# Performance work log

Hardware: AMD Instinct MI355X
Metric: run time of the kernel (lower is better)

## Reference

```python
import jax, jax.numpy as jnp
import numpy as np

N, E, CS, HE, H = 10000, 160000, 128, 32, 4
S0, V1 = 16, 8          # feat_irreps = 16x0e + 8x1o
QK0, QK1 = 4, 2         # qk_irreps per head = 4x0e + 2x1o
VO0, VO1 = 4, 4         # v_irreps  per head = 4x0e + 4x1o
OK0, OK1 = QK0 * H, QK1 * H     # 16, 8
OV0, OV1 = VO0 * H, VO1 * H     # 16, 16
K_NUMEL = S0*OK0 + V1*OK0 + S0*OK1 + V1*OK1 + V1*OK1   # 640
V_NUMEL = S0*OV0 + V1*OV0 + S0*OV1 + V1*OV1 + V1*OV1   # 896
EPS = 1e-5


def _tp(fs, fv, sh_s, sh_v, w, o0, o1):
    """CG tensor product of (s0 scalars + v1 vectors) with sh=(1x0e+1x1o),
    per-edge weights w (shared_weights=False); outputs o0 scalars + o1 vectors.
    Paths: 0e*0e->0e, 1o.1o->0e (dot), 0e*1o->1o, 1o*0e->1o, 1o x 1o->1o (cross)."""
    s0, v1 = fs.shape[-1], fv.shape[-2]
    i = 0
    ws = []
    for (a, b) in ((s0, o0), (v1, o0), (s0, o1), (v1, o1), (v1, o1)):
        ws.append(w[:, i:i + a * b].reshape(-1, a, b)); i += a * b
    wA, wB, wC, wD, wE = ws
    c0a = jnp.einsum('eu,euw->ew', fs * sh_s[:, None], wA) / np.sqrt(s0)
    dv = jnp.einsum('eui,ei->eu', fv, sh_v)
    c0b = jnp.einsum('eu,euw->ew', dv, wB) / np.sqrt(v1)
    out0 = (c0a + c0b) / np.sqrt(2.0)
    c1c = jnp.einsum('eu,euw->ew', fs, wC)[:, :, None] * sh_v[:, None, :] / np.sqrt(s0)
    c1d = jnp.einsum('eui,euw->ewi', fv, wD) * sh_s[:, None, None] / np.sqrt(v1)
    crs = jnp.cross(fv, sh_v[:, None, :])
    c1e = jnp.einsum('eui,euw->ewi', crs, wE) / np.sqrt(v1)
    out1 = (c1c + c1d + c1e) / np.sqrt(3.0)
    return out0, out1


def _forward(frame_features, rigid_rot, rigid_trans, tfn_features, edge_features, edge_sh,
             W_f0, b_f0, W_f1, b_f1, Wg_s, Wg_v, Wq_s, Wq_v,
             Wk1, bk1, Wk2, bk2, Wv1, bv1, Wv2, bv2,
             Wo_s, Wo_v, Ws_s, Ws_v, bn_ws, bn_bs, bn_wv, edge_index):
    dst, src = edge_index[0], edge_index[1]
    n = tfn_features.shape[0]
    tfn_s = tfn_features[:, :S0]
    tfn_v = tfn_features[:, S0:].reshape(n, V1, 3)
    sh_s, sh_v = edge_sh[:, 0], edge_sh[:, 1:4]

    # frame -> irrep features: 0e via Linear, 1o via Linear + rigid apply
    f0 = frame_features @ W_f0 + b_f0                                   # [N, S0*H]
    f1 = (frame_features @ W_f1 + b_f1).reshape(n, V1 * H, 3)
    f1 = jnp.einsum('nij,nuj->nui', rigid_rot, f1) + rigid_trans[:, None, :]
    gs = f0 @ Wg_s / np.sqrt(f0.shape[-1])                              # o3.Linear 0e -> [N, S0]
    gv = jnp.einsum('nui,uw->nwi', f1, Wg_v) / np.sqrt(f1.shape[1])     # o3.Linear 1o -> [N, V1, 3]

    # queries per node, per head
    q_s = (tfn_s @ Wq_s / np.sqrt(S0)).reshape(n, H, QK0)
    q_v = (jnp.einsum('nui,uw->nwi', tfn_v, Wq_v) / np.sqrt(V1)).reshape(n, H, QK1, 3)

    # per-edge dynamic TP weights from edge features (the big memory term)
    kw = jax.nn.relu(edge_features @ Wk1 + bk1) @ Wk2 + bk2             # [E, 640]
    vw = jax.nn.relu(edge_features @ Wv1 + bv1) @ Wv2 + bv2             # [E, 896]

    fs, fv = gs[dst], gv[dst]                                           # gather at edge_dst
    k_s, k_v = _tp(fs, fv, sh_s, sh_v, kw, OK0, OK1)
    v_s, v_v = _tp(fs, fv, sh_s, sh_v, vw, OV0, OV1)
    k_s = k_s.reshape(-1, H, QK0); k_v = k_v.reshape(-1, H, QK1, 3)
    v_s = v_s.reshape(-1, H, VO0); v_v = v_v.reshape(-1, H, VO1, 3)

    # attention scores + segment softmax over edge_src groups
    attn = jnp.einsum('ehj,ehj->eh', q_s[src], k_s) + jnp.einsum('ehji,ehji->eh', q_v[src], k_v)
    m = jax.ops.segment_max(attn, src, num_segments=n)
    ex = jnp.exp(attn - m[src])
    den = jax.ops.segment_sum(ex, src, num_segments=n)
    alpha = ex / (den[src] + 1e-9)

    upd_s = jax.ops.segment_sum(v_s * alpha[..., None], src, num_segments=n).reshape(n, OV0)
    upd_v = jax.ops.segment_sum(v_v * alpha[..., None, None], src, num_segments=n).reshape(n, OV1, 3)

    out_s = upd_s @ Wo_s / np.sqrt(OV0) + tfn_s @ Ws_s / np.sqrt(S0)
    out_v = jnp.einsum('nui,uw->nwi', upd_v, Wo_v) / np.sqrt(OV1) \
          + jnp.einsum('nui,uw->nwi', tfn_v, Ws_v) / np.sqrt(V1)

    # e3nn-style BatchNorm: scalars mean/var normalized, vectors norm normalized
    mu = out_s.mean(0); xc = out_s - mu
    out_s = xc / jnp.sqrt((xc * xc).mean(0) + EPS) * bn_ws + bn_bs
    n2 = (out_v * out_v).sum(-1).mean(0)
    out_v = out_v / jnp.sqrt(n2 + EPS)[None, :, None] * bn_wv[None, :, None]

    return jnp.concatenate([out_s, out_v.reshape(n, V1 * 3)], axis=-1)   # [N, 40]


def setup_inputs():
    key = jax.random.key(0)
    ks = iter(jax.random.split(key, 40))
    rn = lambda *s: jax.random.normal(next(ks), s, dtype=jnp.float32)
    return dict(
        frame_features=rn(N, CS),
        rigid_rot=rn(N, 3, 3),
        rigid_trans=rn(N, 3),
        tfn_features=rn(N, S0 + 3 * V1),
        edge_features=rn(E, HE),
        edge_sh=rn(E, 4),
        edge_index=jax.random.randint(next(ks), (2, E), 0, N, dtype=jnp.int32),
        W_f0=rn(CS, S0 * H) / np.sqrt(CS), b_f0=jnp.zeros((S0 * H,), jnp.float32),
        W_f1=rn(CS, V1 * H * 3) / np.sqrt(CS), b_f1=jnp.zeros((V1 * H * 3,), jnp.float32),
        Wg_s=rn(S0 * H, S0), Wg_v=rn(V1 * H, V1),
        Wq_s=rn(S0, QK0 * H), Wq_v=rn(V1, QK1 * H),
        Wk1=rn(HE, HE) / np.sqrt(HE), bk1=jnp.zeros((HE,), jnp.float32),
        Wk2=rn(HE, K_NUMEL) / np.sqrt(HE), bk2=jnp.zeros((K_NUMEL,), jnp.float32),
        Wv1=rn(HE, HE) / np.sqrt(HE), bv1=jnp.zeros((HE,), jnp.float32),
        Wv2=rn(HE, V_NUMEL) / np.sqrt(HE), bv2=jnp.zeros((V_NUMEL,), jnp.float32),
        Wo_s=rn(VO0 * H, S0), Wo_v=rn(VO1 * H, V1),
        Ws_s=rn(S0, S0), Ws_v=rn(V1, V1),
        bn_ws=jnp.ones((S0,), jnp.float32), bn_bs=jnp.zeros((S0,), jnp.float32),
        bn_wv=jnp.ones((V1,), jnp.float32),
    )


def reference(frame_features, rigid_rot, rigid_trans, tfn_features, edge_features, edge_sh, edge_index,
              W_f0, b_f0, W_f1, b_f1, Wg_s, Wg_v, Wq_s, Wq_v,
              Wk1, bk1, Wk2, bk2, Wv1, bv1, Wv2, bv2,
              Wo_s, Wo_v, Ws_s, Ws_v, bn_ws, bn_bs, bn_wv):
    return _forward(frame_features, rigid_rot, rigid_trans, tfn_features, edge_features, edge_sh,
                    W_f0, b_f0, W_f1, b_f1, Wg_s, Wg_v, Wq_s, Wq_v,
                    Wk1, bk1, Wk2, bk2, Wv1, bv1, Wv2, bv2,
                    Wo_s, Wo_v, Ws_s, Ws_v, bn_ws, bn_bs, bn_wv, edge_index)
```

## Files before the change

### kernel.cpp

```cpp
#include <hip/hip_runtime.h>
#include <hip/hip_bf16.h>
#include <math.h>

#define NN 10000
#define EE 160000
#define CSZ 128
#define NVB (EE/128)

#define INV_S8  0.35355339059327373f
#define INV_S32 0.17677669529663687f
#define INV_S2  0.7071067811865476f
#define INV_S3  0.5773502691896258f

typedef short s16x8 __attribute__((ext_vector_type(8)));
typedef float f32x4 __attribute__((ext_vector_type(4)));

__device__ __forceinline__ unsigned short f2bf(float f){
  __hip_bfloat16 h = __float2bfloat16(f);
  return *reinterpret_cast<unsigned short*>(&h);
}

__global__ __launch_bounds__(192) void k_node(
    const float* __restrict__ frame,
    const float* __restrict__ Wf0, const float* __restrict__ bf0,
    const float* __restrict__ Wf1, const float* __restrict__ bf1,
    const float* __restrict__ rot, const float* __restrict__ trans,
    const float* __restrict__ tfn,
    const float* __restrict__ Wgs, const float* __restrict__ Wgv,
    const float* __restrict__ Wqs, const float* __restrict__ Wqv,
    float* __restrict__ Gs, float* __restrict__ Gv,
    float* __restrict__ Qs, float* __restrict__ Qv){
  __shared__ float ff[160];
  __shared__ float f1r[32][3];
  int n = blockIdx.x;
  int t = threadIdx.x;
  if(t < 160){
    bool is0 = t < 64;
    int cc = is0 ? t : (t-64);
    const float* W = is0 ? Wf0 : Wf1;
    int ldw = is0 ? 64 : 96;
    float acc = is0 ? bf0[cc] : bf1[cc];
    const float* fp = frame + (size_t)n*CSZ;
    #pragma unroll 8
    for(int k=0;k<CSZ;k++)
      acc = fmaf(fp[k], W[k*ldw + cc], acc);
    ff[t] = acc;
  }
  __syncthreads();
  if(t < 32){
    float v0 = ff[64+t*3+0], v1 = ff[64+t*3+1], v2 = ff[64+t*3+2];
    const float* R = rot + (size_t)n*9;
    const float* tr = trans + (size_t)n*3;
    f1r[t][0] = R[0]*v0 + R[1]*v1 + R[2]*v2 + tr[0];
    f1r[t][1] = R[3]*v0 + R[4]*v1 + R[5]*v2 + tr[1];
    f1r[t][2] = R[6]*v0 + R[7]*v1 + R[8]*v2 + tr[2];
  }
  __syncthreads();
  if(t < 16){
    float a = 0.f;
    #pragma unroll
    for(int u=0;u<64;u++) a = fmaf(ff[u], Wgs[u*16+t], a);
    Gs[(size_t)n*16+t] = a * 0.125f;
  } else if(t < 40){
    int idx = t-16, w = idx/3, i = idx%3; float a = 0.f;
    #pragma unroll
    for(int u=0;u<32;u++) a = fmaf(f1r[u][i], Wgv[u*8+w], a);
    Gv[(size_t)n*24+idx] = a * INV_S32;
  } else if(t < 56){
    int w = t-40; float a = 0.f;
    #pragma unroll
    for(int u=0;u<16;u++) a = fmaf(tfn[(size_t)n*40+u], Wqs[u*16+w], a);
    Qs[(size_t)n*16+w] = a * 0.25f;
  } else if(t < 80){
    int idx = t-56, w = idx/3, i = idx%3; float a = 0.f;
    #pragma unroll
    for(int u=0;u<8;u++) a = fmaf(tfn[(size_t)n*40+16+u*3+i], Wqv[u*8+w], a);
    Qv[(size_t)n*24+idx] = a * INV_S8;
  }
}

__global__ __launch_bounds__(256) void k_hist(const int* __restrict__ ei, int* __restrict__ cnt){
  int e = blockIdx.x*256 + threadIdx.x;
  if(e < EE) atomicAdd(&cnt[ei[EE + e]], 1);
}

__global__ __launch_bounds__(256) void k_scan(const int* __restrict__ cnt,
                                              int* __restrict__ ofs, int* __restrict__ fill){
  __shared__ int tsum[256];
  int t = threadIdx.x;
  const int CH = (NN + 255)/256;
  int base = t*CH;
  int s = 0;
  for(int i=0;i<CH;i++){ int idx=base+i; if(idx<NN) s += cnt[idx]; }
  tsum[t] = s;
  __syncthreads();
  for(int off=1; off<256; off<<=1){
    int v = (t>=off)? tsum[t-off] : 0;
    __syncthreads();
    tsum[t] += v;
    __syncthreads();
  }
  int run = (t==0)? 0 : tsum[t-1];
  for(int i=0;i<CH;i++){
    int idx = base+i;
    if(idx < NN){ ofs[idx] = run; fill[idx] = run; run += cnt[idx]; }
  }
  if(t==255) ofs[NN] = tsum[255];
}

__global__ __launch_bounds__(256) void k_scatter(const int* __restrict__ ei,
                                                 int* __restrict__ fill, int* __restrict__ elist){
  int e = blockIdx.x*256 + threadIdx.x;
  if(e >= EE) return;
  int src = ei[EE + e];
  int pos = atomicAdd(&fill[src], 1);
  elist[pos] = e;
}

__global__ __launch_bounds__(256) void k_prepw(
    const float* __restrict__ Wk2, const float* __restrict__ bk2,
    const float* __restrict__ Wv2, const float* __restrict__ bv2,
    unsigned short* __restrict__ A2rK, unsigned short* __restrict__ A2rV,
    float* __restrict__ biasK, float* __restrict__ biasV){
  int tid = blockIdx.x*256 + threadIdx.x;
  const int NV = 896*32, NK = 640*32;
  if(tid < NV){
    int c = tid>>5, h = tid&31;
    float s = (c<384)? INV_S2 : INV_S3;
    A2rV[(c>>4)*512 + (c&15)*32 + h] = f2bf(Wv2[h*896+c]*s);
  } else if(tid < NV+NK){
    int i = tid - NV; int c = i>>5, h = i&31;
    float s = (c<384)? INV_S2 : INV_S3;
    A2rK[(c>>4)*512 + (c&15)*32 + h] = f2bf(Wk2[h*640+c]*s);
  } else if(tid < NV+NK+896){
    int c = tid - (NV+NK);
    biasV[c] = bv2[c] * ((c<384)? INV_S2 : INV_S3);
  } else if(tid < NV+NK+896+640){
    int c = tid - (NV+NK+896);
    biasK[c] = bk2[c] * ((c<384)? INV_S2 : INV_S3);
  }
}

#define HID_TO_FRAGS(W1, b1) { \
  unsigned short* hL = (unsigned short*)&F[0][0]; \
  float efv[32]; \
  const float4* efp = (const float4*)(ef + (size_t)e*32); \
  _Pragma("unroll") \
  for(int q=0;q<8;q++){ float4 t=efp[q]; efv[q*4]=t.x; efv[q*4+1]=t.y; efv[q*4+2]=t.z; efv[q*4+3]=t.w; } \
  float hd[32]; \
  _Pragma("unroll") \
  for(int h=0;h<32;h++) hd[h] = b1[h]; \
  _Pragma("unroll") \
  for(int k=0;k<32;k++){ \
    float ekv = efv[k]; \
    _Pragma("unroll") \
    for(int h=0;h<32;h++) hd[h] = fmaf(ekv, W1[k*32+h], hd[h]); \
  } \
  _Pragma("unroll") \
  for(int gg=0;gg<4;gg++){ \
    s16x8 p; \
    _Pragma("unroll") \
    for(int j=0;j<8;j++) p[j] = (short)f2bf(fmaxf(hd[gg*8+j], 0.f)); \
    *(s16x8*)&hL[((g*4+gg)*16 + e16)*8] = p; \
  } \
  _Pragma("unroll") \
  for(int tt=0;tt<4;tt++) \
    af[tt] = *(const s16x8*)&hL[((tt*4 + g)*16 + e16)*8]; }

#define STAGE_FEATURES() { \
  const float4* g4 = (const float4*)(Gs + (size_t)dst*16); \
  _Pragma("unroll") \
  for(int q=0;q<4;q++){ float4 t = g4[q]; \
    F[q*4+0][lane]=t.x*0.25f; F[q*4+1][lane]=t.y*0.25f; \
    F[q*4+2][lane]=t.z*0.25f; F[q*4+3][lane]=t.w*0.25f; } \
  const float4* v4 = (const float4*)(Gv + (size_t)dst*24); \
  _Pragma("unroll") \
  for(int q=0;q<6;q++){ float4 t = v4[q]; \
    F[16+q*4+0][lane]=t.x; F[16+q*4+1][lane]=t.y; \
    F[16+q*4+2][lane]=t.z; F[16+q*4+3][lane]=t.w; } \
  _Pragma("unroll") \
  for(int tt=0;tt<4;tt++){ \
    int sl = tt*16 + e16; \
    shs_t[tt]  = __shfl(shs, sl); \
    sv_t[tt][0]= __shfl(sv0, sl); \
    sv_t[tt][1]= __shfl(sv1, sl); \
    sv_t[tt][2]= __shfl(sv2, sl); \
    shsI8_t[tt]= shs_t[tt]*INV_S8; \
  } }

#define PIPE_LOOP(A2r, bias, FIRST, LAST, ...) { \
  s16x8 Aw = *(const s16x8*)&A2r[(FIRST)*512 + e16*32 + g*8]; \
  float4 b4 = *(const float4*)&bias[(FIRST)*16 + g*4]; \
  _Pragma("unroll 2") \
  for(int ntile=(FIRST); ntile<(LAST); ++ntile){ \
    int ntp = (ntile+1 < (LAST))? ntile+1 : ntile; \
    s16x8 Awn = *(const s16x8*)&A2r[ntp*512 + e16*32 + g*8]; \
    float4 b4n = *(const float4*)&bias[ntp*16 + g*4]; \
    f32x4 acc4[4]; \
    _Pragma("unroll") \
    for(int tt=0; tt<4; ++tt){ \
      f32x4 a0 = {b4.x, b4.y, b4.z, b4.w}; \
      acc4[tt] = __builtin_amdgcn_mfma_f32_16x16x32_bf16(Aw, af[tt], a0, 0, 0, 0); \
    } \
    __VA_ARGS__ \
    Aw = Awn; b4 = b4n; \
  } }

__device__ __forceinline__ void edge_v_body(
    int blk, float (*F)[64],
    const int* __restrict__ ei, const float* __restrict__ esh,
    const float* __restrict__ ef,
    const float* __restrict__ Gs, const float* __restrict__ Gv,
    const float* __restrict__ Wv1, const float* __restrict__ bv1,
    const unsigned short* __restrict__ A2rV, const float* __restrict__ biasV,
    float* __restrict__ EdgeV){
  int wave = threadIdx.x >> 6, lane = threadIdx.x & 63;
  int ebase = blk*128 + wave*64;
  int e = ebase + lane;
  int e16 = lane & 15, g = lane >> 4;

  int dst = ei[e];
  float4 sh4 = *(const float4*)(esh + (size_t)e*4);
  float shs = sh4.x, sv0 = sh4.y, sv1 = sh4.z, sv2 = sh4.w;

  s16x8 af[4];
  HID_TO_FRAGS(Wv1, bv1);
  float shs_t[4], sv_t[4][3], shsI8_t[4];
  STAGE_FEATURES();

  float A16[4][4] = {};
  PIPE_LOOP(A2rV, biasV, 0, 16,
    _Pragma("unroll")
    for(int tt=0; tt<4; ++tt){
      float f = F[ntile][tt*16+e16] * shs_t[tt];
      _Pragma("unroll")
      for(int r=0;r<4;r++) A16[tt][r] = fmaf(f, acc4[tt][r], A16[tt][r]);
    }
  );
  PIPE_LOOP(A2rV, biasV, 16, 24,
    int u3 = 16 + (ntile-16)*3;
    _Pragma("unroll")
    for(int tt=0; tt<4; ++tt){
      int eL = tt*16+e16;
      float f = (F[u3+0][eL]*sv_t[tt][0] + F[u3+1][eL]*sv_t[tt][1]
               + F[u3+2][eL]*sv_t[tt][2]) * INV_S8;
      _Pragma("unroll")
      for(int r=0;r<4;r++) A16[tt][r] = fmaf(f, acc4[tt][r], A16[tt][r]);
    }
  );
  #pragma unroll
  for(int tt=0; tt<4; ++tt){
    int eo = ebase + tt*16 + e16;
    *(float4*)(EdgeV + (size_t)eo*64 + g*4) =
        make_float4(A16[tt][0], A16[tt][1], A16[tt][2], A16[tt][3]);
  }

  float VV[4][4][3] = {};
  PIPE_LOOP(A2rV, biasV, 24, 40,
    _Pragma("unroll")
    for(int tt=0; tt<4; ++tt){
      float f = F[ntile-24][tt*16+e16];
      _Pragma("unroll")
      for(int r=0;r<4;r++){
        float c = f*acc4[tt][r];
        VV[tt][r][0] = fmaf(c, sv_t[tt][0], VV[tt][r][0]);
        VV[tt][r][1] = fmaf(c, sv_t[tt][1], VV[tt][r][1]);
        VV[tt][r][2] = fmaf(c, sv_t[tt][2], VV[tt][r][2]);
      }
    }
  );
  PIPE_LOOP(A2rV, biasV, 40, 48,
    int u3 = 16 + (ntile-40)*3;
    _Pragma("unroll")
    for(int tt=0; tt<4; ++tt){
      int eL = tt*16+e16;
      float f0 = F[u3+0][eL]*shsI8_t[tt];
      float f1 = F[u3+1][eL]*shsI8_t[tt];
      float f2 = F[u3+2][eL]*shsI8_t[tt];
      _Pragma("unroll")
      for(int r=0;r<4;r++){
        VV[tt][r][0] = fmaf(f0, acc4[tt][r], VV[tt][r][0]);
        VV[tt][r][1] = fmaf(f1, acc4[tt][r], VV[tt][r][1]);
        VV[tt][r][2] = fmaf(f2, acc4[tt][r], VV[tt][r][2]);
      }
    }
  );
  PIPE_LOOP(A2rV, biasV, 48, 56,
    int u3 = 16 + (ntile-48)*3;
    _Pragma("unroll")
    for(int tt=0; tt<4; ++tt){
      int eL = tt*16+e16;
      float a0 = F[u3+0][eL], a1 = F[u3+1][eL], a2 = F[u3+2][eL];
      float x0 = (a1*sv_t[tt][2] - a2*sv_t[tt][1])*INV_S8;
      float x1 = (a2*sv_t[tt][0] - a0*sv_t[tt][2])*INV_S8;
      float x2 = (a0*sv_t[tt][1] - a1*sv_t[tt][0])*INV_S8;
      _Pragma("unroll")
      for(int r=0;r<4;r++){
        VV[tt][r][0] = fmaf(x0, acc4[tt][r], VV[tt][r][0]);
        VV[tt][r][1] = fmaf(x1, acc4[tt][r], VV[tt][r][1]);
        VV[tt][r][2] = fmaf(x2, acc4[tt][r], VV[tt][r][2]);
      }
    }
  );
  #pragma unroll
  for(int tt=0; tt<4; ++tt){
    int eo = ebase + tt*16 + e16;
    float* op = EdgeV + (size_t)eo*64 + 16 + g*12;
    float v[12] = {VV[tt][0][0],VV[tt][0][1],VV[tt][0][2],
                   VV[tt][1][0],VV[tt][1][1],VV[tt][1][2],
                   VV[tt][2][0],VV[tt][2][1],VV[tt][2][2],
                   VV[tt][3][0],VV[tt][3][1],VV[tt][3][2]};
    #pragma unroll
    for(int k=0;k<6;k++)
      *(float2*)(op + k*2) = make_float2(v[k*2], v[k*2+1]);
  }
}

__device__ __forceinline__ void edge_k_body(
    int blk, float (*F)[64],
    const int* __restrict__ ei, const float* __restrict__ esh,
    const float* __restrict__ ef,
    const float* __restrict__ Gs, const float* __restrict__ Gv,
    const float* __restrict__ Qs, const float* __restrict__ Qv,
    const float* __restrict__ Wk1, const float* __restrict__ bk1,
    const unsigned short* __restrict__ A2rK, const float* __restrict__ biasK,
    float* __restrict__ Attn){
  int wave = threadIdx.x >> 6, lane = threadIdx.x & 63;
  int ebase = blk*128 + wave*64;
  int e = ebase + lane;
  int e16 = lane & 15, g = lane >> 4;

  int dst = ei[e];
  float4 sh4 = *(const float4*)(esh + (size_t)e*4);
  float shs = sh4.x, sv0 = sh4.y, sv1 = sh4.z, sv2 = sh4.w;

  s16x8 af[4];
  HID_TO_FRAGS(Wk1, bk1);
  float shs_t[4], sv_t[4][3], shsI8_t[4];
  STAGE_FEATURES();

  float KS[4][4] = {};
  PIPE_LOOP(A2rK, biasK, 0, 16,
    _Pragma("unroll")
    for(int tt=0; tt<4; ++tt){
      float f = F[ntile][tt*16+e16] * shs_t[tt];
      _Pragma("unroll")
      for(int r=0;r<4;r++) KS[tt][r] = fmaf(f, acc4[tt][r], KS[tt][r]);
    }
  );
  PIPE_LOOP(A2rK, biasK, 16, 24,
    int u3 = 16 + (ntile-16)*3;
    _Pragma("unroll")
    for(int tt=0; tt<4; ++tt){
      int eL = tt*16+e16;
      float f = (F[u3+0][eL]*sv_t[tt][0] + F[u3+1][eL]*sv_t[tt][1]
               + F[u3+2][eL]*sv_t[tt][2]) * INV_S8;
      _Pragma("unroll")
      for(int r=0;r<4;r++) KS[tt][r] = fmaf(f, acc4[tt][r], KS[tt][r]);
    }
  );
  int src_t[4]; float ksd[4];
  #pragma unroll
  for(int tt=0; tt<4; ++tt){
    int eo = ebase + tt*16 + e16;
    src_t[tt] = ei[EE + eo];
    float4 q4 = *(const float4*)(Qs + (size_t)src_t[tt]*16 + g*4);
    ksd[tt] = q4.x*KS[tt][0] + q4.y*KS[tt][1] + q4.z*KS[tt][2] + q4.w*KS[tt][3];
  }

  float KV[4][4][3] = {};
  int gh = g >> 1;
  PIPE_LOOP(A2rK, biasK, 24, 32,
    int fr = (ntile-24)*2 + gh;
    _Pragma("unroll")
    for(int tt=0; tt<4; ++tt){
      float f = F[fr][tt*16+e16];
      _Pragma("unroll")
      for(int r=0;r<4;r++){
        float c = f*acc4[tt][r];
        KV[tt][r][0] = fmaf(c, sv_t[tt][0], KV[tt][r][0]);
        KV[tt][r][1] = fmaf(c, sv_t[tt][1], KV[tt][r][1]);
        KV[tt][r][2] = fmaf(c, sv_t[tt][2], KV[tt][r][2]);
      }
    }
  );
  PIPE_LOOP(A2rK, biasK, 32, 36,
    int u3 = 16 + ((ntile-32)*2 + gh)*3;
    _Pragma("unroll")
    for(int tt=0; tt<4; ++tt){
      int eL = tt*16+e16;
      float f0 = F[u3+0][eL]*shsI8_t[tt];
      float f1 = F[u3+1][eL]*shsI8_t[tt];
      float f2 = F[u3+2][eL]*shsI8_t[tt];
      _Pragma("unroll")
      for(int r=0;r<4;r++){
        KV[tt][r][0] = fmaf(f0, acc4[tt][r], KV[tt][r][0]);
        KV[tt][r][1] = fmaf(f1, acc4[tt][r], KV[tt][r][1]);
        KV[tt][r][2] = fmaf(f2, acc4[tt][r], KV[tt][r][2]);
      }
    }
  );
  PIPE_LOOP(A2rK, biasK, 36, 40,
    int u3 = 16 + ((ntile-36)*2 + gh)*3;
    _Pragma("unroll")
    for(int tt=0; tt<4; ++tt){
      int eL = tt*16+e16;
      float a0 = F[u3+0][eL], a1 = F[u3+1][eL], a2 = F[u3+2][eL];
      float x0 = (a1*sv_t[tt][2] - a2*sv_t[tt][1])*INV_S8;
      float x1 = (a2*sv_t[tt][0] - a0*sv_t[tt][2])*INV_S8;
      float x2 = (a0*sv_t[tt][1] - a1*sv_t[tt][0])*INV_S8;
      _Pragma("unroll")
      for(int r=0;r<4;r++){
        KV[tt][r][0] = fmaf(x0, acc4[tt][r], KV[tt][r][0]);
        KV[tt][r][1] = fmaf(x1, acc4[tt][r], KV[tt][r][1]);
        KV[tt][r][2] = fmaf(x2, acc4[tt][r], KV[tt][r][2]);
      }
    }
  );
  int godd = g & 1;
  #pragma unroll
  for(int tt=0; tt<4; ++tt){
    const float* qvp = Qv + (size_t)src_t[tt]*24 + godd*12;
    float4 qa = *(const float4*)(qvp);
    float4 qb = *(const float4*)(qvp+4);
    float4 qc = *(const float4*)(qvp+8);
    float kvs0 = qa.x*KV[tt][0][0] + qa.y*KV[tt][0][1] + qa.z*KV[tt][0][2]
               + qa.w*KV[tt][1][0] + qb.x*KV[tt][1][1] + qb.y*KV[tt][1][2];
    float kvs1 = qb.z*KV[tt][2][0] + qb.w*KV[tt][2][1] + qc.x*KV[tt][2][2]
               + qc.y*KV[tt][3][0] + qc.z*KV[tt][3][1] + qc.w*KV[tt][3][2];
    float p0 = ((g==0)? ksd[tt] : 0.f) + (godd? 0.f : kvs0);
    float p1 = ((g==1)? ksd[tt] : 0.f) + (godd? 0.f : kvs1);
    float p2 = ((g==2)? ksd[tt] : 0.f) + (godd? kvs0 : 0.f);
    float p3 = ((g==3)? ksd[tt] : 0.f) + (godd? kvs1 : 0.f);
    p0 += __shfl_xor(p0,16); p0 += __shfl_xor(p0,32);
    p1 += __shfl_xor(p1,16); p1 += __shfl_xor(p1,32);
    p2 += __shfl_xor(p2,16); p2 += __shfl_xor(p2,32);
    p3 += __shfl_xor(p3,16); p3 += __shfl_xor(p3,32);
    if(lane < 16){
      int eo = ebase + tt*16 + lane;
      *(float4*)(Attn + (size_t)eo*4) = make_float4(p0, p1, p2, p3);
    }
  }
}

__global__ __launch_bounds__(128) void k_edge_vk(
    const int* __restrict__ ei, const float* __restrict__ esh,
    const float* __restrict__ ef,
    const float* __restrict__ Gs, const float* __restrict__ Gv,
    const float* __restrict__ Qs, const float* __restrict__ Qv,
    const float* __restrict__ Wv1, const float* __restrict__ bv1,
    const float* __restrict__ Wk1, const float* __restrict__ bk1,
    const unsigned short* __restrict__ A2rV, const float* __restrict__ biasV,
    const unsigned short* __restrict__ A2rK, const float* __restrict__ biasK,
    float* __restrict__ EdgeV, float* __restrict__ Attn){
  __shared__ float featAll[2][40][64];
  float (*F)[64] = featAll[threadIdx.x >> 6];
  if(blockIdx.x < NVB)
    edge_v_body(blockIdx.x, F, ei, esh, ef, Gs, Gv, Wv1, bv1, A2rV, biasV, EdgeV);
  else
    edge_k_body(blockIdx.x - NVB, F, ei, esh, ef, Gs, Gv, Qs, Qv, Wk1, bk1, A2rK, biasK, Attn);
}

__global__ __launch_bounds__(256) void k_reduce(
    const int* __restrict__ ofs, const int* __restrict__ elist,
    const float* __restrict__ Attn, const float* __restrict__ EdgeV,
    float* __restrict__ Upd){
  int wid = threadIdx.x >> 6, ln = threadIdx.x & 63;
  int n = blockIdx.x*4 + wid;
  if(n >= NN) return;
  int beg = ofs[n], end = ofs[n+1];
  float m0=-3.4e38f, m1=-3.4e38f, m2=-3.4e38f, m3=-3.4e38f;
  for(int i=beg+ln; i<end; i+=64){
    int e = elist[i];
    float4 a = *(const float4*)(Attn + (size_t)e*4);
    m0=fmaxf(m0,a.x); m1=fmaxf(m1,a.y); m2=fmaxf(m2,a.z); m3=fmaxf(m3,a.w);
  }
  #pragma unroll
  for(int off=1; off<64; off<<=1){
    m0=fmaxf(m0,__shfl_xor(m0,off)); m1=fmaxf(m1,__shfl_xor(m1,off));
    m2=fmaxf(m2,__shfl_xor(m2,off)); m3=fmaxf(m3,__shfl_xor(m3,off));
  }
  int h = (ln < 16) ? (ln >> 2) : (((ln - 16)/3) >> 2);
  float mh = (h==0)?m0:(h==1)?m1:(h==2)?m2:m3;
  float acc = 0.f, den = 0.f;
  for(int i=beg; i<end; i++){
    int e = elist[i];
    float v  = EdgeV[(size_t)e*64 + ln];
    float a  = Attn[(size_t)e*4 + h];
    float ex = __expf(a - mh);
    acc = fmaf(ex, v, acc);
    den += ex;
  }
  Upd[(size_t)n*64 + ln] = acc / (den + 1e-9f);
}

__global__ __launch_bounds__(256) void k_nodeout(
    const float* __restrict__ Upd, const float* __restrict__ tfn,
    const float* __restrict__ Wos, const float* __restrict__ Wov,
    const float* __restrict__ Wss, const float* __restrict__ Wsv,
    float* __restrict__ Pre){
  int idx = blockIdx.x*256 + threadIdx.x;
  if(idx >= NN*40) return;
  int n = idx/40, c = idx - n*40;
  const float* up = Upd + (size_t)n*64;
  const float* tp = tfn + (size_t)n*40;
  float out;
  if(c < 16){
    float a=0.f, b=0.f;
    #pragma unroll
    for(int u=0;u<16;u++){
      a = fmaf(up[u], Wos[u*16+c], a);
      b = fmaf(tp[u], Wss[u*16+c], b);
    }
    out = (a+b)*0.25f;
  } else {
    int w = (c-16)/3, i = (c-16)%3;
    float a=0.f, b=0.f;
    #pragma unroll
    for(int u=0;u<16;u++) a = fmaf(up[16+u*3+i], Wov[u*8+w], a);
    #pragma unroll
    for(int u=0;u<8;u++)  b = fmaf(tp[16+u*3+i], Wsv[u*8+w], b);
    out = a*0.25f + b*INV_S8;
  }
  Pre[idx] = out;
}

__global__ __launch_bounds__(256) void k_stats(
    const float* __restrict__ Pre, float* __restrict__ Stats){
  int b = blockIdx.x;
  int lane = threadIdx.x & 63, wave = threadIdx.x >> 6;
  float s1 = 0.f, s2 = 0.f;
  if(b < 16){
    for(int n = threadIdx.x; n < NN; n += 256){
      float x = Pre[(size_t)n*40 + b];
      s1 += x; s2 += x*x;
    }
  } else {
    int w3 = 16 + (b-16)*3;
    for(int n = threadIdx.x; n < NN; n += 256){
      const float* p = Pre + (size_t)n*40 + w3;
      s1 += p[0]*p[0] + p[1]*p[1] + p[2]*p[2];
    }
  }
  #pragma unroll
  for(int off=1; off<64; off<<=1){
    s1 += __shfl_xor(s1, off);
    s2 += __shfl_xor(s2, off);
  }
  __shared__ float ws1[4], ws2[4];
  if(lane == 0){ ws1[wave] = s1; ws2[wave] = s2; }
  __syncthreads();
  if(threadIdx.x == 0){
    float t1 = ws1[0]+ws1[1]+ws1[2]+ws1[3];
    float t2 = ws2[0]+ws2[1]+ws2[2]+ws2[3];
    if(b < 16){ Stats[b] = t1; Stats[16+b] = t2; }
    else        Stats[32+(b-16)] = t1;
  }
}

__global__ __launch_bounds__(256) void k_final(
    const float* __restrict__ Pre, const float* __restrict__ Stats,
    const float* __restrict__ bnws, const float* __restrict__ bnbs,
    const float* __restrict__ bnwv, float* __restrict__ Out){
  int idx = blockIdx.x*256 + threadIdx.x;
  if(idx >= NN*40) return;
  int n = idx/40, c = idx - n*40;
  float x = Pre[idx];
  float r;
  if(c < 16){
    float mu  = Stats[c]    * (1.f/NN);
    float var = Stats[16+c] * (1.f/NN) - mu*mu;
    r = (x - mu) / sqrtf(var + 1e-5f) * bnws[c] + bnbs[c];
  } else {
    int w = (c-16)/3;
    float n2 = Stats[32+w] * (1.f/NN);
    r = x / sqrtf(n2 + 1e-5f) * bnwv[w];
  }
  Out[idx] = r;
}

extern "C" void kernel_launch(void* const* d_in, const int* in_sizes, int n_in,
                              void* d_out, int out_size, void* d_ws, size_t ws_size,
                              hipStream_t stream){
  const float* frame = (const float*)d_in[0];
  const float* rot   = (const float*)d_in[1];
  const float* trans = (const float*)d_in[2];
  const float* tfn   = (const float*)d_in[3];
  const float* ef    = (const float*)d_in[4];
  const float* esh   = (const float*)d_in[5];
  const int*   ei    = (const int*)  d_in[6];
  const float* Wf0   = (const float*)d_in[7];
  const float* bf0   = (const float*)d_in[8];
  const float* Wf1   = (const float*)d_in[9];
  const float* bf1   = (const float*)d_in[10];
  const float* Wgs   = (const float*)d_in[11];
  const float* Wgv   = (const float*)d_in[12];
  const float* Wqs   = (const float*)d_in[13];
  const float* Wqv   = (const float*)d_in[14];
  const float* Wk1   = (const float*)d_in[15];
  const float* bk1   = (const float*)d_in[16];
  const float* Wk2   = (const float*)d_in[17];
  const float* bk2   = (const float*)d_in[18];
  const float* Wv1   = (const float*)d_in[19];
  const float* bv1   = (const float*)d_in[20];
  const float* Wv2   = (const float*)d_in[21];
  const float* bv2   = (const float*)d_in[22];
  const float* Wos   = (const float*)d_in[23];
  const float* Wov   = (const float*)d_in[24];
  const float* Wss   = (const float*)d_in[25];
  const float* Wsv   = (const float*)d_in[26];
  const float* bnws  = (const float*)d_in[27];
  const float* bnbs  = (const float*)d_in[28];
  const float* bnwv  = (const float*)d_in[29];

  float* ws   = (float*)d_ws;
  float* f0f1 = ws;
  float* Gs   = f0f1 + (size_t)NN*160;
  float* Gv   = Gs   + (size_t)NN*16;
  float* Qs   = Gv   + (size_t)NN*24;
  float* Qv   = Qs   + (size_t)NN*16;
  float* Attn = Qv   + (size_t)NN*24;
  float* Pre  = Attn + (size_t)EE*4;
  float* Upd  = Pre  + (size_t)NN*40;
  float* EdgeV= Upd  + (size_t)NN*64;
  float* Stats= EdgeV+ (size_t)EE*64;
  int*   cnt  = (int*)(Stats + 64);
  int*   ofs  = cnt + (NN+16);
  int*   fill = ofs + (NN+16);
  int*   elist= fill + (NN+16);
  float* biasV= (float*)(elist + EE);
  float* biasK= biasV + 896;
  unsigned short* A2rV = (unsigned short*)(biasK + 640);
  unsigned short* A2rK = A2rV + 896*32;

  hipMemsetAsync(cnt, 0, (NN + 16)*sizeof(int), stream);

  k_node    <<<dim3(NN),              192, 0, stream>>>(frame, Wf0, bf0, Wf1, bf1,
                                                        rot, trans, tfn,
                                                        Wgs, Wgv, Wqs, Wqv,
                                                        Gs, Gv, Qs, Qv);
  k_prepw   <<<dim3(198),             256, 0, stream>>>(Wk2, bk2, Wv2, bv2, A2rK, A2rV, biasK, biasV);
  k_hist    <<<dim3((EE+255)/256),    256, 0, stream>>>(ei, cnt);
  k_scan    <<<dim3(1),               256, 0, stream>>>(cnt, ofs, fill);
  k_scatter <<<dim3((EE+255)/256),    256, 0, stream>>>(ei, fill, elist);
  k_edge_vk <<<dim3(2*NVB),           128, 0, stream>>>(ei, esh, ef, Gs, Gv, Qs, Qv,
                                                        Wv1, bv1, Wk1, bk1,
                                                        A2rV, biasV, A2rK, biasK,
                                                        EdgeV, Attn);
  k_reduce  <<<dim3((NN+3)/4),        256, 0, stream>>>(ofs, elist, Attn, EdgeV, Upd);
  k_nodeout <<<dim3((NN*40+255)/256), 256, 0, stream>>>(Upd, tfn, Wos, Wov, Wss, Wsv, Pre);
  k_stats   <<<dim3(24),              256, 0, stream>>>(Pre, Stats);
  k_final   <<<dim3((NN*40+255)/256), 256, 0, stream>>>(Pre, Stats, bnws, bnbs, bnwv, (float*)d_out);
}
```

Measured before the change: 281.8 us.

## Stage per-edge weight tiles in double-buffered LDS shared by four waves

```diff
diff --git a/kernel.cpp b/kernel.cpp
--- a/kernel.cpp
+++ b/kernel.cpp
@@ -5,7 +5,7 @@
 #define NN 10000
 #define EE 160000
 #define CSZ 128
-#define NVB (EE/128)
+#define NVB (EE/256)
 
 #define INV_S8  0.35355339059327373f
 #define INV_S32 0.17677669529663687f
@@ -188,26 +188,49 @@
     shsI8_t[tt]= shs_t[tt]*INV_S8; \
   } }
 
-#define PIPE_LOOP(A2r, bias, FIRST, LAST, ...) { \
-  s16x8 Aw = *(const s16x8*)&A2r[(FIRST)*512 + e16*32 + g*8]; \
-  float4 b4 = *(const float4*)&bias[(FIRST)*16 + g*4]; \
-  _Pragma("unroll 2") \
-  for(int ntile=(FIRST); ntile<(LAST); ++ntile){ \
-    int ntp = (ntile+1 < (LAST))? ntile+1 : ntile; \
-    s16x8 Awn = *(const s16x8*)&A2r[ntp*512 + e16*32 + g*8]; \
-    float4 b4n = *(const float4*)&bias[ntp*16 + g*4]; \
-    f32x4 acc4[4]; \
+#define STAGE_ISSUE(A2r, bias, C0) do{ \
+  wreg = *(const float4*)((const char*)(A2r) + (size_t)(C0)*1024 + (size_t)threadIdx.x*16); \
+  if(threadIdx.x < 64) breg = (bias)[(C0)*16 + threadIdx.x]; \
+}while(0)
+
+#define STAGE_WRITE(WB, BB) do{ \
+  *(float4*)((char*)(WB) + (size_t)threadIdx.x*16) = wreg; \
+  if(threadIdx.x < 64) (BB)[threadIdx.x] = breg; \
+}while(0)
+
+#define LDS_PIPE(A2r, bias, FIRST, LAST, ...) { \
+  float4 wreg; float breg = 0.f; \
+  STAGE_ISSUE(A2r, bias, FIRST); \
+  STAGE_WRITE(wbuf[0], bbuf[0]); \
+  __syncthreads(); \
+  int cur = 0; \
+  _Pragma("unroll 1") \
+  for(int c0=(FIRST); c0<(LAST); c0+=4){ \
+    bool more = (c0+4) < (LAST); \
+    if(more){ STAGE_ISSUE(A2r, bias, c0+4); } \
+    const unsigned short* wb = wbuf[cur]; \
+    const float* bb = bbuf[cur]; \
     _Pragma("unroll") \
-    for(int tt=0; tt<4; ++tt){ \
-      f32x4 a0 = {b4.x, b4.y, b4.z, b4.w}; \
-      acc4[tt] = __builtin_amdgcn_mfma_f32_16x16x32_bf16(Aw, af[tt], a0, 0, 0, 0); \
+    for(int nt=0; nt<4; ++nt){ \
+      int ntile = c0 + nt; \
+      s16x8 Aw = *(const s16x8*)&wb[nt*512 + e16*32 + g*8]; \
+      float4 b4 = *(const float4*)&bb[nt*16 + g*4]; \
+      f32x4 acc4[4]; \
+      _Pragma("unroll") \
+      for(int tt=0; tt<4; ++tt){ \
+        f32x4 a0 = {b4.x, b4.y, b4.z, b4.w}; \
+        acc4[tt] = __builtin_amdgcn_mfma_f32_16x16x32_bf16(Aw, af[tt], a0, 0, 0, 0); \
+      } \
+      __VA_ARGS__ \
     } \
-    __VA_ARGS__ \
-    Aw = Awn; b4 = b4n; \
+    if(more){ STAGE_WRITE(wbuf[cur^1], bbuf[cur^1]); } \
+    __syncthreads(); \
+    cur ^= 1; \
   } }
 
 __device__ __forceinline__ void edge_v_body(
     int blk, float (*F)[64],
+    unsigned short (*wbuf)[2048], float (*bbuf)[64],
     const int* __restrict__ ei, const float* __restrict__ esh,
     const float* __restrict__ ef,
     const float* __restrict__ Gs, const float* __restrict__ Gv,
@@ -215,7 +238,7 @@
     const unsigned short* __restrict__ A2rV, const float* __restrict__ biasV,
     float* __restrict__ EdgeV){
   int wave = threadIdx.x >> 6, lane = threadIdx.x & 63;
-  int ebase = blk*128 + wave*64;
+  int ebase = blk*256 + wave*64;
   int e = ebase + lane;
   int e16 = lane & 15, g = lane >> 4;
 
@@ -229,7 +252,7 @@
   STAGE_FEATURES();
 
   float A16[4][4] = {};
-  PIPE_LOOP(A2rV, biasV, 0, 16,
+  LDS_PIPE(A2rV, biasV, 0, 16,
     _Pragma("unroll")
     for(int tt=0; tt<4; ++tt){
       float f = F[ntile][tt*16+e16] * shs_t[tt];
@@ -237,7 +260,7 @@
       for(int r=0;r<4;r++) A16[tt][r] = fmaf(f, acc4[tt][r], A16[tt][r]);
     }
   );
-  PIPE_LOOP(A2rV, biasV, 16, 24,
+  LDS_PIPE(A2rV, biasV, 16, 24,
     int u3 = 16 + (ntile-16)*3;
     _Pragma("unroll")
     for(int tt=0; tt<4; ++tt){
@@ -256,7 +279,7 @@
   }
 
   float VV[4][4][3] = {};
-  PIPE_LOOP(A2rV, biasV, 24, 40,
+  LDS_PIPE(A2rV, biasV, 24, 40,
     _Pragma("unroll")
     for(int tt=0; tt<4; ++tt){
       float f = F[ntile-24][tt*16+e16];
@@ -269,7 +292,7 @@
       }
     }
   );
-  PIPE_LOOP(A2rV, biasV, 40, 48,
+  LDS_PIPE(A2rV, biasV, 40, 48,
     int u3 = 16 + (ntile-40)*3;
     _Pragma("unroll")
     for(int tt=0; tt<4; ++tt){
@@ -285,7 +308,7 @@
       }
     }
   );
-  PIPE_LOOP(A2rV, biasV, 48, 56,
+  LDS_PIPE(A2rV, biasV, 48, 56,
     int u3 = 16 + (ntile-48)*3;
     _Pragma("unroll")
     for(int tt=0; tt<4; ++tt){
@@ -318,6 +341,7 @@
 
 __device__ __forceinline__ void edge_k_body(
     int blk, float (*F)[64],
+    unsigned short (*wbuf)[2048], float (*bbuf)[64],
     const int* __restrict__ ei, const float* __restrict__ esh,
     const float* __restrict__ ef,
     const float* __restrict__ Gs, const float* __restrict__ Gv,
@@ -326,7 +350,7 @@
     const unsigned short* __restrict__ A2rK, const float* __restrict__ biasK,
     float* __restrict__ Attn){
   int wave = threadIdx.x >> 6, lane = threadIdx.x & 63;
-  int ebase = blk*128 + wave*64;
+  int ebase = blk*256 + wave*64;
   int e = ebase + lane;
   int e16 = lane & 15, g = lane >> 4;
 
@@ -340,7 +364,7 @@
   STAGE_FEATURES();
 
   float KS[4][4] = {};
-  PIPE_LOOP(A2rK, biasK, 0, 16,
+  LDS_PIPE(A2rK, biasK, 0, 16,
     _Pragma("unroll")
     for(int tt=0; tt<4; ++tt){
       float f = F[ntile][tt*16+e16] * shs_t[tt];
@@ -348,7 +372,7 @@
       for(int r=0;r<4;r++) KS[tt][r] = fmaf(f, acc4[tt][r], KS[tt][r]);
     }
   );
-  PIPE_LOOP(A2rK, biasK, 16, 24,
+  LDS_PIPE(A2rK, biasK, 16, 24,
     int u3 = 16 + (ntile-16)*3;
     _Pragma("unroll")
     for(int tt=0; tt<4; ++tt){
@@ -370,7 +394,7 @@
 
   float KV[4][4][3] = {};
   int gh = g >> 1;
-  PIPE_LOOP(A2rK, biasK, 24, 32,
+  LDS_PIPE(A2rK, biasK, 24, 32,
     int fr = (ntile-24)*2 + gh;
     _Pragma("unroll")
     for(int tt=0; tt<4; ++tt){
@@ -384,36 +408,37 @@
       }
     }
   );
-  PIPE_LOOP(A2rK, biasK, 32, 36,
-    int u3 = 16 + ((ntile-32)*2 + gh)*3;
-    _Pragma("unroll")
-    for(int tt=0; tt<4; ++tt){
-      int eL = tt*16+e16;
-      float f0 = F[u3+0][eL]*shsI8_t[tt];
-      float f1 = F[u3+1][eL]*shsI8_t[tt];
-      float f2 = F[u3+2][eL]*shsI8_t[tt];
-      _Pragma("unroll")
-      for(int r=0;r<4;r++){
-        KV[tt][r][0] = fmaf(f0, acc4[tt][r], KV[tt][r][0]);
-        KV[tt][r][1] = fmaf(f1, acc4[tt][r], KV[tt][r][1]);
-        KV[tt][r][2] = fmaf(f2, acc4[tt][r], KV[tt][r][2]);
+  LDS_PIPE(A2rK, biasK, 32, 40,
+    if(ntile < 36){
+      int u3 = 16 + ((ntile-32)*2 + gh)*3;
+      _Pragma("unroll")
+      for(int tt=0; tt<4; ++tt){
+        int eL = tt*16+e16;
+        float f0 = F[u3+0][eL]*shsI8_t[tt];
+        float f1 = F[u3+1][eL]*shsI8_t[tt];
+        float f2 = F[u3+2][eL]*shsI8_t[tt];
+        _Pragma("unroll")
+        for(int r=0;r<4;r++){
+          KV[tt][r][0] = fmaf(f0, acc4[tt][r], KV[tt][r][0]);
+          KV[tt][r][1] = fmaf(f1, acc4[tt][r], KV[tt][r][1]);
+          KV[tt][r][2] = fmaf(f2, acc4[tt][r], KV[tt][r][2]);
+        }
       }
-    }
-  );
-  PIPE_LOOP(A2rK, biasK, 36, 40,
-    int u3 = 16 + ((ntile-36)*2 + gh)*3;
-    _Pragma("unroll")
-    for(int tt=0; tt<4; ++tt){
-      int eL = tt*16+e16;
-      float a0 = F[u3+0][eL], a1 = F[u3+1][eL], a2 = F[u3+2][eL];
-      float x0 = (a1*sv_t[tt][2] - a2*sv_t[tt][1])*INV_S8;
-      float x1 = (a2*sv_t[tt][0] - a0*sv_t[tt][2])*INV_S8;
-      float x2 = (a0*sv_t[tt][1] - a1*sv_t[tt][0])*INV_S8;
-      _Pragma("unroll")
-      for(int r=0;r<4;r++){
-        KV[tt][r][0] = fmaf(x0, acc4[tt][r], KV[tt][r][0]);
-        KV[tt][r][1] = fmaf(x1, acc4[tt][r], KV[tt][r][1]);
-        KV[tt][r][2] = fmaf(x2, acc4[tt][r], KV[tt][r][2]);
+    } else {
+      int u3 = 16 + ((ntile-36)*2 + gh)*3;
+      _Pragma("unroll")
+      for(int tt=0; tt<4; ++tt){
+        int eL = tt*16+e16;
+        float a0 = F[u3+0][eL], a1 = F[u3+1][eL], a2 = F[u3+2][eL];
+        float x0 = (a1*sv_t[tt][2] - a2*sv_t[tt][1])*INV_S8;
+        float x1 = (a2*sv_t[tt][0] - a0*sv_t[tt][2])*INV_S8;
+        float x2 = (a0*sv_t[tt][1] - a1*sv_t[tt][0])*INV_S8;
+        _Pragma("unroll")
+        for(int r=0;r<4;r++){
+          KV[tt][r][0] = fmaf(x0, acc4[tt][r], KV[tt][r][0]);
+          KV[tt][r][1] = fmaf(x1, acc4[tt][r], KV[tt][r][1]);
+          KV[tt][r][2] = fmaf(x2, acc4[tt][r], KV[tt][r][2]);
+        }
       }
     }
   );
@@ -443,7 +468,7 @@
   }
 }
 
-__global__ __launch_bounds__(128) void k_edge_vk(
+__global__ __launch_bounds__(256) void k_edge_vk(
     const int* __restrict__ ei, const float* __restrict__ esh,
     const float* __restrict__ ef,
     const float* __restrict__ Gs, const float* __restrict__ Gv,
@@ -453,12 +478,14 @@
     const unsigned short* __restrict__ A2rV, const float* __restrict__ biasV,
     const unsigned short* __restrict__ A2rK, const float* __restrict__ biasK,
     float* __restrict__ EdgeV, float* __restrict__ Attn){
-  __shared__ float featAll[2][40][64];
+  __shared__ float featAll[4][40][64];
+  __shared__ unsigned short wbuf[2][2048];
+  __shared__ float bbuf[2][64];
   float (*F)[64] = featAll[threadIdx.x >> 6];
   if(blockIdx.x < NVB)
-    edge_v_body(blockIdx.x, F, ei, esh, ef, Gs, Gv, Wv1, bv1, A2rV, biasV, EdgeV);
+    edge_v_body(blockIdx.x, F, wbuf, bbuf, ei, esh, ef, Gs, Gv, Wv1, bv1, A2rV, biasV, EdgeV);
   else
-    edge_k_body(blockIdx.x - NVB, F, ei, esh, ef, Gs, Gv, Qs, Qv, Wk1, bk1, A2rK, biasK, Attn);
+    edge_k_body(blockIdx.x - NVB, F, wbuf, bbuf, ei, esh, ef, Gs, Gv, Qs, Qv, Wk1, bk1, A2rK, biasK, Attn);
 }
 
 __global__ __launch_bounds__(256) void k_reduce(
@@ -643,7 +670,7 @@
   k_hist    <<<dim3((EE+255)/256),    256, 0, stream>>>(ei, cnt);
   k_scan    <<<dim3(1),               256, 0, stream>>>(cnt, ofs, fill);
   k_scatter <<<dim3((EE+255)/256),    256, 0, stream>>>(ei, fill, elist);
-  k_edge_vk <<<dim3(2*NVB),           128, 0, stream>>>(ei, esh, ef, Gs, Gv, Qs, Qv,
+  k_edge_vk <<<dim3(2*NVB),           256, 0, stream>>>(ei, esh, ef, Gs, Gv, Qs, Qv,
                                                         Wv1, bv1, Wk1, bk1,
                                                         A2rV, biasV, A2rK, biasK,
                                                         EdgeV, Attn);
```

After: 268.4 us. 4.8% less time.
